# Kernel optimization log

Hardware: AMD Instinct MI355X
Metric: run time of the kernel (lower is better)

Reference implementation:

```python
import jax, jax.numpy as jnp
import numpy as np

N = 50000   # num_entities
R = 16      # num_relations
B = 8       # num_bases
D = 128     # embedding_dim == hidden_dim
E = 625000  # num_edges
EPS = 1e-5  # LayerNorm eps


def _rgcn_layer(x, row, col, edge_type, bases, coef, selfw, bias):
    # weights[r] = sum_b coef[r,b] * bases[b]  (rio). We apply bases to x first
    # (cheaper: N*B*d*d) then mix by coefficients, since (x @ W[r])[col] == x[col] @ W[r].
    z = jnp.einsum('ni,bio->bno', x, bases)          # [B,N,D]
    y = jnp.einsum('rb,bno->rno', coef, z)           # [R,N,D] == x @ W[r]
    msg = y[edge_type, col]                          # [E,D] per-edge messages
    key = edge_type * N + row                        # combined (relation,node) segment id
    agg = jax.ops.segment_sum(msg, key, num_segments=R * N).reshape(R, N, D)
    deg = jax.ops.segment_sum(jnp.ones((msg.shape[0],), x.dtype), key,
                              num_segments=R * N).reshape(R, N, 1)
    agg = (agg / jnp.maximum(deg, 1.0)).sum(0)       # per-relation mean-agg, summed over r
    return x @ selfw + agg + bias


def _layernorm(x, g, b):
    m = x.mean(-1, keepdims=True)
    v = ((x - m) ** 2).mean(-1, keepdims=True)
    return (x - m) * jax.lax.rsqrt(v + EPS) * g + b


def setup_inputs() -> dict:
    key = jax.random.key(0)
    ks = jax.random.split(key, 10)
    s = 1.0 / np.sqrt(D)
    sb = 1.0 / np.sqrt(B)
    return {
        'edge_index': jax.random.randint(ks[0], (2, E), 0, N),
        'edge_type': jax.random.randint(ks[1], (E,), 0, R),
        'emb': jax.random.normal(ks[2], (N, D), jnp.float32) * s,
        'bases1': jax.random.normal(ks[3], (B, D, D), jnp.float32) * s,
        'coef1': jax.random.normal(ks[4], (R, B), jnp.float32) * sb,
        'selfw1': jax.random.normal(ks[5], (D, D), jnp.float32) * s,
        'bias1': jnp.zeros((D,), jnp.float32),
        'g1': jnp.ones((D,), jnp.float32),
        'b1': jnp.zeros((D,), jnp.float32),
        'bases2': jax.random.normal(ks[6], (B, D, D), jnp.float32) * s,
        'coef2': jax.random.normal(ks[7], (R, B), jnp.float32) * sb,
        'selfw2': jax.random.normal(ks[8], (D, D), jnp.float32) * s,
        'bias2': jnp.zeros((D,), jnp.float32),
        'g2': jnp.ones((D,), jnp.float32),
        'b2': jnp.zeros((D,), jnp.float32),
    }


def reference(edge_index, edge_type, emb, bases1, coef1, selfw1, bias1, g1, b1,
              bases2, coef2, selfw2, bias2, g2, b2):
    row, col = edge_index[0], edge_index[1]
    x = emb
    # layer 1 (dropout is identity in eval)
    x = _rgcn_layer(x, row, col, edge_type, bases1, coef1, selfw1, bias1)
    x = jax.nn.relu(_layernorm(x, g1, b1))
    # layer 2
    x = _rgcn_layer(x, row, col, edge_type, bases2, coef2, selfw2, bias2)
    x = jax.nn.relu(_layernorm(x, g2, b2))
    return x
```

## Files before the change

### kernel.cpp

```cpp
#include <hip/hip_runtime.h>
#include <hip/hip_bf16.h>


static constexpr int kDim = 128;
static constexpr int kRel = 16;
static constexpr int kBas = 8;
static constexpr int kSeg = kBas + 1;

typedef __attribute__((ext_vector_type(8))) short bf16x8;
typedef __attribute__((ext_vector_type(4))) float f32x4;

static __device__ __forceinline__ float bf2f_rg(unsigned short h) {
    return __uint_as_float(((unsigned)h) << 16);
}
static __device__ __forceinline__ unsigned short f2bf_rg(float f) {
    unsigned u = __float_as_uint(f);
    u = u + 0x7fffu + ((u >> 16) & 1u);
    return (unsigned short)(u >> 16);
}

static __device__ __forceinline__ void gload_lds16(const void* g, void* l) {
    __builtin_amdgcn_global_load_lds(
        (const __attribute__((address_space(1))) unsigned*)g,
        (__attribute__((address_space(3))) unsigned*)l, 16, 0, 0);
}

static __device__ __forceinline__ int flag_from(const unsigned short* x, int lane) {
    unsigned e0 = ((unsigned)x[lane] >> 7) & 0xFFu;
    unsigned e1 = ((unsigned)x[lane + 64] >> 7) & 0xFFu;
    int bad = (e0 >= 0x86u) || (e1 >= 0x86u);
    return (__ballot(bad) != 0ull) ? 1 : 0;
}

__global__ void RGCNEncoder_89962384982025_kernel(unsigned* p, int n) {
    int i = blockIdx.x * 256 + threadIdx.x;
    if (i < n) p[i] = 0x3F803F80u;
}

__global__ void cvt_rg(const void* xraw, unsigned short* xout, int n) {
    __shared__ int fsh;
    if (threadIdx.x < 64) {
        int fl = flag_from((const unsigned short*)xraw, threadIdx.x);
        if (threadIdx.x == 0) fsh = fl;
    }
    __syncthreads();
    int f = fsh;
    int i = blockIdx.x * 256 + threadIdx.x;
    if (i >= n) return;
    if (f)
        xout[i] = f2bf_rg(((const float*)xraw)[i]);
    else
        xout[i] = ((const unsigned short*)xraw)[i];
}

__global__ void zero_rg(int* p, int n) {
    int i = blockIdx.x * 256 + threadIdx.x;
    if (i < n) p[i] = 0;
}

__global__ void count_rg(const int* ei, const int* et, int* cnt, int E) {
    int e = blockIdx.x * 256 + threadIdx.x;
    if (e < E) atomicAdd(&cnt[ei[e] * kRel + et[e]], 1);
}

__global__ void scanA_rg(const int* cnt, int* rowptr, int* bsum, int n) {
    __shared__ int sh[256];
    int tid = threadIdx.x;
    int i = blockIdx.x * 256 + tid;
    int v = (i < n) ? cnt[i] : 0;
    sh[tid] = v;
    __syncthreads();
    for (int off = 1; off < 256; off <<= 1) {
        int t = (tid >= off) ? sh[tid - off] : 0;
        __syncthreads();
        sh[tid] += t;
        __syncthreads();
    }
    if (i < n) rowptr[i + 1] = sh[tid];
    if (tid == 255) bsum[blockIdx.x] = sh[255];
}
__global__ void scanB_rg(int* bsum, int nb) {
    __shared__ int partial[256];
    int tid = threadIdx.x;
    int chunk = (nb + 255) / 256;
    int s0 = tid * chunk;
    int s1 = min(s0 + chunk, nb);
    int sum = 0;
    for (int i = s0; i < s1; ++i) sum += bsum[i];
    partial[tid] = sum;
    __syncthreads();
    for (int off = 1; off < 256; off <<= 1) {
        int t = (tid >= off) ? partial[tid - off] : 0;
        __syncthreads();
        partial[tid] += t;
        __syncthreads();
    }
    int run = (tid == 0) ? 0 : partial[tid - 1];
    for (int i = s0; i < s1; ++i) { int v = bsum[i]; bsum[i] = run; run += v; }
}
__global__ void scanC_rg(int* rowptr, const int* bsum, int n) {
    int i = blockIdx.x * 256 + threadIdx.x;
    if (i < n) rowptr[i + 1] += bsum[blockIdx.x];
    if (i == 0) rowptr[0] = 0;
}

__global__ void fill_rg(const int* ei, const int* et, const int* rowptr,
                        int* cnt, int* pcols, int E) {
    int e = blockIdx.x * 256 + threadIdx.x;
    if (e < E) {
        int rel = et[e];
        int key = ei[e] * kRel + rel;
        int old = atomicSub(&cnt[key], 1);
        pcols[rowptr[key] + old - 1] = ei[E + e] | (rel << 26);
    }
}

__global__ void wall_rg(const void* bases, const void* coef, const void* selfw,
                        const unsigned short* emb, unsigned short* wallT,
                        float* coefw) {
    __shared__ int fsh;
    if (threadIdx.x < 64) {
        int fl = flag_from(emb, threadIdx.x);
        if (threadIdx.x == 0) fsh = fl;
    }
    __syncthreads();
    int f = fsh;
    int idx = blockIdx.x * 256 + threadIdx.x;
    int b = idx >> 14;
    int o = (idx >> 7) & 127;
    int k = idx & 127;
    if (blockIdx.x == 0 && threadIdx.x < kRel * kBas) {
        coefw[threadIdx.x] = f ? ((const float*)coef)[threadIdx.x]
                               : bf2f_rg(((const unsigned short*)coef)[threadIdx.x]);
    }
    if (b < kBas) {
        float bv = f ? ((const float*)bases)[b * 16384 + k * 128 + o]
                     : bf2f_rg(((const unsigned short*)bases)[b * 16384 + k * 128 + o]);
        wallT[idx] = f2bf_rg(bv);
    } else {
        float sv = f ? ((const float*)selfw)[k * 128 + o]
                     : bf2f_rg(((const unsigned short*)selfw)[k * 128 + o]);
        wallT[idx] = f2bf_rg(sv);
    }
}

__global__ __launch_bounds__(256) void agg2_rg(const int* rowptr2, const int* pcols,
                                               const unsigned short* xsrc,
                                               const float* coefw,
                                               unsigned short* Gall, int N) {
    __shared__ float csh[kRel * kBas];
    if (threadIdx.x < kRel * kBas) csh[threadIdx.x] = coefw[threadIdx.x];
    __syncthreads();
    int wv = threadIdx.x >> 6;
    int lane = threadIdx.x & 63;
    int n = blockIdx.x * 4 + wv;
    if (n >= N) return;
    const int s = rowptr2[n * kRel];
    const int e = rowptr2[n * kRel + kRel];
    const unsigned short* xl = xsrc + 2 * lane;
    float g0[kBas], g1[kBas];
#pragma unroll
    for (int b = 0; b < kBas; ++b) { g0[b] = 0.f; g1[b] = 0.f; }
    float s0 = 0.f, s1 = 0.f;
    int cur = -1, cnt = 0;
    auto flush = [&]() {
        float w = __builtin_amdgcn_rcpf((float)cnt);
        float t0 = s0 * w, t1 = s1 * w;
        const float* cr = csh + cur * kBas;
#pragma unroll
        for (int b = 0; b < kBas; ++b) {
            float c = cr[b];
            g0[b] += c * t0;
            g1[b] += c * t1;
        }
        s0 = 0.f; s1 = 0.f; cnt = 0;
    };
    for (int base = s; base < e; base += 64) {
        int m = e - base;
        if (m > 64) m = 64;
        int pk = 0;
        if (base + lane < e) pk = pcols[base + lane];
        int i = 0;
        for (; i + 4 <= m; i += 4) {
            int v0 = __builtin_amdgcn_readlane(pk, i);
            int v1 = __builtin_amdgcn_readlane(pk, i + 1);
            int v2 = __builtin_amdgcn_readlane(pk, i + 2);
            int v3 = __builtin_amdgcn_readlane(pk, i + 3);
            unsigned u0 = *(const unsigned*)(xl + (size_t)(v0 & 0x03FFFFFF) * 128);
            unsigned u1 = *(const unsigned*)(xl + (size_t)(v1 & 0x03FFFFFF) * 128);
            unsigned u2 = *(const unsigned*)(xl + (size_t)(v2 & 0x03FFFFFF) * 128);
            unsigned u3 = *(const unsigned*)(xl + (size_t)(v3 & 0x03FFFFFF) * 128);
            int r0 = (int)((unsigned)v0 >> 26);
            int r1 = (int)((unsigned)v1 >> 26);
            int r2 = (int)((unsigned)v2 >> 26);
            int r3 = (int)((unsigned)v3 >> 26);
            if (r0 != cur) { if (cnt) flush(); cur = r0; }
            s0 += __uint_as_float(u0 << 16); s1 += __uint_as_float(u0 & 0xffff0000u); ++cnt;
            if (r1 != cur) { flush(); cur = r1; }
            s0 += __uint_as_float(u1 << 16); s1 += __uint_as_float(u1 & 0xffff0000u); ++cnt;
            if (r2 != cur) { flush(); cur = r2; }
            s0 += __uint_as_float(u2 << 16); s1 += __uint_as_float(u2 & 0xffff0000u); ++cnt;
            if (r3 != cur) { flush(); cur = r3; }
            s0 += __uint_as_float(u3 << 16); s1 += __uint_as_float(u3 & 0xffff0000u); ++cnt;
        }
        for (; i < m; ++i) {
            int v = __builtin_amdgcn_readlane(pk, i);
            unsigned u = *(const unsigned*)(xl + (size_t)(v & 0x03FFFFFF) * 128);
            int rel = (int)((unsigned)v >> 26);
            if (rel != cur) { if (cnt) flush(); cur = rel; }
            s0 += __uint_as_float(u << 16);
            s1 += __uint_as_float(u & 0xffff0000u);
            ++cnt;
        }
    }
    if (cnt) flush();
    unsigned short* grow = Gall + (size_t)n * (kBas * 128) + 2 * lane;
#pragma unroll
    for (int b = 0; b < kBas; ++b) {
        unsigned outp = (unsigned)f2bf_rg(g0[b]) | ((unsigned)f2bf_rg(g1[b]) << 16);
        *(unsigned*)(grow + b * 128) = outp;
    }
}

__global__ __launch_bounds__(256, 3) void fusegemm_rg(const unsigned short* Gall,
                                                      const unsigned short* x,
                                                      const unsigned short* wallT,
                                                      const void* bias, const void* gw,
                                                      const void* bw,
                                                      const unsigned short* emb,
                                                      unsigned short* out_b, float* out_f,
                                                      int ofp32, int M) {
    __shared__ __align__(16) unsigned short As[2][64][128];
    __shared__ float pS[64][5];
    __shared__ float pQ[64][5];
    __shared__ float mrs[64][2];
    __shared__ int fsh;
    const int m0 = blockIdx.x * 64;
    const int tid = threadIdx.x;
    const int wave = tid >> 6;
    const int lane = tid & 63;
    const int wn = wave * 32;
    const int lrow = lane & 15;
    const int lq = lane >> 4;
    if (tid < 64) {
        int fl = flag_from(emb, tid);
        if (tid == 0) fsh = fl;
    }

    auto stage = [&](int seg, int buf) {
        const char* srcb;
        size_t rstrideB, segoffB;
        if (seg < kBas) { srcb = (const char*)Gall; rstrideB = kBas * 256; segoffB = (size_t)seg * 256; }
        else            { srcb = (const char*)x;    rstrideB = 256;        segoffB = 0; }
#pragma unroll
        for (int it = 0; it < 4; ++it) {
            int gi = (wave * 4 + it) * 64 + lane;
            int row = gi >> 4;
            int c = ((gi & 15) << 4) ^ ((row & 7) << 4);
            int gr = m0 + row;
            if (gr > M - 1) gr = M - 1;
            const char* src = srcb + (size_t)gr * rstrideB + segoffB + (size_t)c;
            unsigned short* ldst = &As[buf][0][0] + ((wave * 4 + it) << 9);
            gload_lds16(src, ldst);
        }
    };

    f32x4 acc[4][2] = {};
    stage(0, 0);
    __syncthreads();
    int cur = 0;
    for (int seg = 0; seg < kSeg; ++seg) {
        const unsigned short* Bsrc = wallT + (size_t)seg * 16384;
        bf16x8 b[4][2];
#pragma unroll
        for (int kk4 = 0; kk4 < 4; ++kk4)
#pragma unroll
            for (int nt = 0; nt < 2; ++nt)
                b[kk4][nt] = *(const bf16x8*)(Bsrc + (size_t)(wn + nt * 16 + lrow) * 128
                                              + kk4 * 32 + lq * 8);
        __builtin_amdgcn_sched_barrier(0);
        if (seg < kSeg - 1) stage(seg + 1, cur ^ 1);
#pragma unroll
        for (int kk4 = 0; kk4 < 4; ++kk4) {
            bf16x8 a4[4];
#pragma unroll
            for (int mt = 0; mt < 4; ++mt) {
                int row = mt * 16 + lrow;
                int cb = (kk4 * 64 + lq * 16) ^ ((row & 7) << 4);
                a4[mt] = *(const bf16x8*)((const char*)&As[cur][0][0]
                                          + row * 256 + cb);
            }
#pragma unroll
            for (int mt = 0; mt < 4; ++mt)
#pragma unroll
                for (int nt = 0; nt < 2; ++nt)
                    acc[mt][nt] = __builtin_amdgcn_mfma_f32_16x16x32_bf16(
                        a4[mt], b[kk4][nt], acc[mt][nt], 0, 0, 0);
        }
        asm volatile("s_waitcnt vmcnt(0)" ::: "memory");
        __builtin_amdgcn_s_barrier();
        cur ^= 1;
    }

    const int f = fsh;
    float bv[2], gv[2], betav[2];
#pragma unroll
    for (int nt = 0; nt < 2; ++nt) {
        int gc = wn + nt * 16 + lrow;
        if (f) {
            bv[nt] = ((const float*)bias)[gc];
            gv[nt] = ((const float*)gw)[gc];
            betav[nt] = ((const float*)bw)[gc];
        } else {
            bv[nt] = bf2f_rg(((const unsigned short*)bias)[gc]);
            gv[nt] = bf2f_rg(((const unsigned short*)gw)[gc]);
            betav[nt] = bf2f_rg(((const unsigned short*)bw)[gc]);
        }
    }
#pragma unroll
    for (int mt = 0; mt < 4; ++mt)
#pragma unroll
        for (int i = 0; i < 4; ++i) {
            float sv = 0.f, qv = 0.f;
#pragma unroll
            for (int nt = 0; nt < 2; ++nt) {
                float v = acc[mt][nt][i] + bv[nt];
                acc[mt][nt][i] = v;
                sv += v;
                qv += v * v;
            }
            for (int o = 1; o < 16; o <<= 1) {
                sv += __shfl_xor(sv, o);
                qv += __shfl_xor(qv, o);
            }
            if (lrow == 0) {
                int row = mt * 16 + lq * 4 + i;
                pS[row][wave] = sv;
                pQ[row][wave] = qv;
            }
        }
    __syncthreads();
    if (tid < 64) {
        float s4 = pS[tid][0] + pS[tid][1] + pS[tid][2] + pS[tid][3];
        float q4 = pQ[tid][0] + pQ[tid][1] + pQ[tid][2] + pQ[tid][3];
        float mean = s4 * (1.0f / 128.0f);
        float var = q4 * (1.0f / 128.0f) - mean * mean;
        mrs[tid][0] = mean;
        mrs[tid][1] = rsqrtf(var + 1e-5f);
    }
    __syncthreads();
#pragma unroll
    for (int mt = 0; mt < 4; ++mt)
#pragma unroll
        for (int i = 0; i < 4; ++i) {
            int row = mt * 16 + lq * 4 + i;
            int gr = m0 + row;
            if (gr < M) {
                float mean = mrs[row][0];
                float rs = mrs[row][1];
#pragma unroll
                for (int nt = 0; nt < 2; ++nt) {
                    int gc = wn + nt * 16 + lrow;
                    float o = fmaxf((acc[mt][nt][i] - mean) * rs * gv[nt] + betav[nt], 0.f);
                    if (ofp32)
                        out_f[(size_t)gr * 128 + gc] = o;
                    else
                        out_b[(size_t)gr * 128 + gc] = f2bf_rg(o);
                }
            }
        }
}

extern "C" void kernel_launch(void* const* d_in, const int* in_sizes, int n_in,
                              void* d_out, int out_size, void* d_ws, size_t ws_size,
                              hipStream_t stream) {
    const int* ei = (const int*)d_in[0];
    const int* et = (const int*)d_in[1];
    const void* emb    = d_in[2];
    const void* bases1 = d_in[3];
    const void* coef1  = d_in[4];
    const void* selfw1 = d_in[5];
    const void* bias1  = d_in[6];
    const void* g1     = d_in[7];
    const void* b1     = d_in[8];
    const void* bases2 = d_in[9];
    const void* coef2  = d_in[10];
    const void* selfw2 = d_in[11];
    const void* bias2  = d_in[12];
    const void* g2     = d_in[13];
    const void* b2     = d_in[14];

    const int E = in_sizes[1];
    const int N = out_size / kDim;
    const int n16 = N * kRel;
    const int nsb = (n16 + 255) / 256;

    char* ws = (char*)d_ws;
    size_t off = 0;
    float* coefw = (float*)(ws + off); off += 512;
    int* rowptr2 = (int*)(ws + off); off += (((size_t)n16 + 1) * 4 + 255) & ~(size_t)255;
    int* cnt     = (int*)(ws + off); off += ((size_t)n16 * 4 + 255) & ~(size_t)255;
    int* bsum    = (int*)(ws + off); off += ((size_t)nsb * 4 + 255) & ~(size_t)255;
    int* pcols   = (int*)(ws + off); off += ((size_t)E * 4 + 255) & ~(size_t)255;
    unsigned short* wallT = (unsigned short*)(ws + off);
    off += ((size_t)kSeg * 16384 * 2 + 255) & ~(size_t)255;
    unsigned short* xin  = (unsigned short*)(ws + off);
    off += ((size_t)N * 128 * 2 + 255) & ~(size_t)255;
    unsigned short* xmid = (unsigned short*)(ws + off);
    off += ((size_t)N * 128 * 2 + 255) & ~(size_t)255;
    unsigned short* Gall = (unsigned short*)(ws + off);
    (void)n_in; (void)ws_size;

    const int eblk = (E + 255) / 256;
    const int mblk64 = (N + 63) / 64;
    const int ablk = (N + 3) / 4;
    const int nelem = N * 128;
    const unsigned short* embh = (const unsigned short*)emb;

    RGCNEncoder_89962384982025_kernel<<<1, 256, 0, stream>>>((unsigned*)d_out, 256);

    cvt_rg<<<(nelem + 255) / 256, 256, 0, stream>>>(emb, xin, nelem);

    zero_rg<<<(n16 + 255) / 256, 256, 0, stream>>>(cnt, n16);
    count_rg<<<eblk, 256, 0, stream>>>(ei, et, cnt, E);
    scanA_rg<<<nsb, 256, 0, stream>>>(cnt, rowptr2, bsum, n16);
    scanB_rg<<<1, 256, 0, stream>>>(bsum, nsb);
    scanC_rg<<<nsb, 256, 0, stream>>>(rowptr2, bsum, n16);
    fill_rg<<<eblk, 256, 0, stream>>>(ei, et, rowptr2, cnt, pcols, E);

    wall_rg<<<kSeg * 64, 256, 0, stream>>>(bases1, coef1, selfw1, embh, wallT, coefw);
    agg2_rg<<<ablk, 256, 0, stream>>>(rowptr2, pcols, xin, coefw, Gall, N);
    fusegemm_rg<<<mblk64, 256, 0, stream>>>(Gall, xin, wallT, bias1, g1, b1, embh,
                                            xmid, (float*)nullptr, 0, N);

    wall_rg<<<kSeg * 64, 256, 0, stream>>>(bases2, coef2, selfw2, embh, wallT, coefw);
    agg2_rg<<<ablk, 256, 0, stream>>>(rowptr2, pcols, xmid, coefw, Gall, N);
    fusegemm_rg<<<mblk64, 256, 0, stream>>>(Gall, xmid, wallT, bias2, g2, b2, embh,
                                            (unsigned short*)nullptr, (float*)d_out,
                                            1, N);
}
```

Baseline: 374.4 us.

## Fuse neighbor aggregation and basis GEMM into one kernel via LDS

Merges the per-node aggregation kernel and the fused GEMM+LayerNorm kernel into one 512-thread kernel per 32-node tile. Each wave aggregates four nodes and writes the per-basis sums straight into swizzled LDS, and the MFMA GEMM then reads them from there. This removes the Gall global intermediate, which costs 8x128 bf16 per node to write and read back, along with one launch per layer. In exchange the block is smaller, the gather phase is serialized within the block before the GEMM starts, and occupancy depends on the larger LDS footprint.

```diff
diff --git a/kernel.cpp b/kernel.cpp
--- a/kernel.cpp
+++ b/kernel.cpp
@@ -144,191 +144,160 @@
     }
 }
 
-__global__ __launch_bounds__(256) void agg2_rg(const int* rowptr2, const int* pcols,
-                                               const unsigned short* xsrc,
-                                               const float* coefw,
-                                               unsigned short* Gall, int N) {
+__global__ __launch_bounds__(512, 4) void aggemm_rg(const int* rowptr2, const int* pcols,
+                                                    const unsigned short* xsrc,
+                                                    const unsigned short* wallT,
+                                                    const float* coefw,
+                                                    const void* bias, const void* gw,
+                                                    const void* bw,
+                                                    const unsigned short* emb,
+                                                    unsigned short* out_b, float* out_f,
+                                                    int ofp32, int M) {
+    __shared__ __align__(16) unsigned short G[kSeg][32][128];
     __shared__ float csh[kRel * kBas];
-    if (threadIdx.x < kRel * kBas) csh[threadIdx.x] = coefw[threadIdx.x];
-    __syncthreads();
-    int wv = threadIdx.x >> 6;
-    int lane = threadIdx.x & 63;
-    int n = blockIdx.x * 4 + wv;
-    if (n >= N) return;
-    const int s = rowptr2[n * kRel];
-    const int e = rowptr2[n * kRel + kRel];
-    const unsigned short* xl = xsrc + 2 * lane;
-    float g0[kBas], g1[kBas];
-#pragma unroll
-    for (int b = 0; b < kBas; ++b) { g0[b] = 0.f; g1[b] = 0.f; }
-    float s0 = 0.f, s1 = 0.f;
-    int cur = -1, cnt = 0;
-    auto flush = [&]() {
-        float w = __builtin_amdgcn_rcpf((float)cnt);
-        float t0 = s0 * w, t1 = s1 * w;
-        const float* cr = csh + cur * kBas;
-#pragma unroll
-        for (int b = 0; b < kBas; ++b) {
-            float c = cr[b];
-            g0[b] += c * t0;
-            g1[b] += c * t1;
-        }
-        s0 = 0.f; s1 = 0.f; cnt = 0;
-    };
-    for (int base = s; base < e; base += 64) {
-        int m = e - base;
-        if (m > 64) m = 64;
-        int pk = 0;
-        if (base + lane < e) pk = pcols[base + lane];
-        int i = 0;
-        for (; i + 4 <= m; i += 4) {
-            int v0 = __builtin_amdgcn_readlane(pk, i);
-            int v1 = __builtin_amdgcn_readlane(pk, i + 1);
-            int v2 = __builtin_amdgcn_readlane(pk, i + 2);
-            int v3 = __builtin_amdgcn_readlane(pk, i + 3);
-            unsigned u0 = *(const unsigned*)(xl + (size_t)(v0 & 0x03FFFFFF) * 128);
-            unsigned u1 = *(const unsigned*)(xl + (size_t)(v1 & 0x03FFFFFF) * 128);
-            unsigned u2 = *(const unsigned*)(xl + (size_t)(v2 & 0x03FFFFFF) * 128);
-            unsigned u3 = *(const unsigned*)(xl + (size_t)(v3 & 0x03FFFFFF) * 128);
-            int r0 = (int)((unsigned)v0 >> 26);
-            int r1 = (int)((unsigned)v1 >> 26);
-            int r2 = (int)((unsigned)v2 >> 26);
-            int r3 = (int)((unsigned)v3 >> 26);
-            if (r0 != cur) { if (cnt) flush(); cur = r0; }
-            s0 += __uint_as_float(u0 << 16); s1 += __uint_as_float(u0 & 0xffff0000u); ++cnt;
-            if (r1 != cur) { flush(); cur = r1; }
-            s0 += __uint_as_float(u1 << 16); s1 += __uint_as_float(u1 & 0xffff0000u); ++cnt;
-            if (r2 != cur) { flush(); cur = r2; }
-            s0 += __uint_as_float(u2 << 16); s1 += __uint_as_float(u2 & 0xffff0000u); ++cnt;
-            if (r3 != cur) { flush(); cur = r3; }
-            s0 += __uint_as_float(u3 << 16); s1 += __uint_as_float(u3 & 0xffff0000u); ++cnt;
-        }
-        for (; i < m; ++i) {
-            int v = __builtin_amdgcn_readlane(pk, i);
-            unsigned u = *(const unsigned*)(xl + (size_t)(v & 0x03FFFFFF) * 128);
-            int rel = (int)((unsigned)v >> 26);
-            if (rel != cur) { if (cnt) flush(); cur = rel; }
-            s0 += __uint_as_float(u << 16);
-            s1 += __uint_as_float(u & 0xffff0000u);
-            ++cnt;
-        }
-    }
-    if (cnt) flush();
-    unsigned short* grow = Gall + (size_t)n * (kBas * 128) + 2 * lane;
-#pragma unroll
-    for (int b = 0; b < kBas; ++b) {
-        unsigned outp = (unsigned)f2bf_rg(g0[b]) | ((unsigned)f2bf_rg(g1[b]) << 16);
-        *(unsigned*)(grow + b * 128) = outp;
-    }
-}
-
-__global__ __launch_bounds__(256, 3) void fusegemm_rg(const unsigned short* Gall,
-                                                      const unsigned short* x,
-                                                      const unsigned short* wallT,
-                                                      const void* bias, const void* gw,
-                                                      const void* bw,
-                                                      const unsigned short* emb,
-                                                      unsigned short* out_b, float* out_f,
-                                                      int ofp32, int M) {
-    __shared__ __align__(16) unsigned short As[2][64][128];
-    __shared__ float pS[64][5];
-    __shared__ float pQ[64][5];
-    __shared__ float mrs[64][2];
+    __shared__ float pS[32][8];
+    __shared__ float pQ[32][8];
+    __shared__ float mrs[32][2];
     __shared__ int fsh;
-    const int m0 = blockIdx.x * 64;
     const int tid = threadIdx.x;
     const int wave = tid >> 6;
     const int lane = tid & 63;
-    const int wn = wave * 32;
-    const int lrow = lane & 15;
-    const int lq = lane >> 4;
+    const int m0 = blockIdx.x * 32;
     if (tid < 64) {
         int fl = flag_from(emb, tid);
         if (tid == 0) fsh = fl;
     }
-
-    auto stage = [&](int seg, int buf) {
-        const char* srcb;
-        size_t rstrideB, segoffB;
-        if (seg < kBas) { srcb = (const char*)Gall; rstrideB = kBas * 256; segoffB = (size_t)seg * 256; }
-        else            { srcb = (const char*)x;    rstrideB = 256;        segoffB = 0; }
-#pragma unroll
-        for (int it = 0; it < 4; ++it) {
-            int gi = (wave * 4 + it) * 64 + lane;
-            int row = gi >> 4;
-            int c = ((gi & 15) << 4) ^ ((row & 7) << 4);
-            int gr = m0 + row;
-            if (gr > M - 1) gr = M - 1;
-            const char* src = srcb + (size_t)gr * rstrideB + segoffB + (size_t)c;
-            unsigned short* ldst = &As[buf][0][0] + ((wave * 4 + it) << 9);
-            gload_lds16(src, ldst);
+    if (tid < kRel * kBas) csh[tid] = coefw[tid];
+
+    {
+        int row = tid >> 4;
+        int c = ((tid & 15) << 4) ^ ((row & 7) << 4);
+        int gr = m0 + row;
+        if (gr > M - 1) gr = M - 1;
+        gload_lds16((const char*)xsrc + (size_t)gr * 256 + c,
+                    &G[kBas][0][0] + tid * 8);
+    }
+    __syncthreads();
+
+    const int ln0 = wave * 4;
+    for (int j = 0; j < 4; ++j) {
+        int ln = ln0 + j;
+        int n = m0 + ln;
+        if (n >= M) break;
+        const int s = rowptr2[n * kRel];
+        const int e = rowptr2[n * kRel + kRel];
+        const unsigned short* xl = xsrc + 2 * lane;
+        float g0[kBas], g1[kBas];
+#pragma unroll
+        for (int b = 0; b < kBas; ++b) { g0[b] = 0.f; g1[b] = 0.f; }
+        float s0 = 0.f, s1 = 0.f;
+        int cur = -1, cnt = 0;
+        auto flush = [&]() {
+            float w = __builtin_amdgcn_rcpf((float)cnt);
+            float t0 = s0 * w, t1 = s1 * w;
+            const float* cr = csh + cur * kBas;
+#pragma unroll
+            for (int b = 0; b < kBas; ++b) {
+                float c = cr[b];
+                g0[b] += c * t0;
+                g1[b] += c * t1;
+            }
+            s0 = 0.f; s1 = 0.f; cnt = 0;
+        };
+        for (int base = s; base < e; base += 64) {
+            int m = e - base;
+            if (m > 64) m = 64;
+            int pk = 0;
+            if (base + lane < e) pk = pcols[base + lane];
+            int i = 0;
+            for (; i + 4 <= m; i += 4) {
+                int v0 = __builtin_amdgcn_readlane(pk, i);
+                int v1 = __builtin_amdgcn_readlane(pk, i + 1);
+                int v2 = __builtin_amdgcn_readlane(pk, i + 2);
+                int v3 = __builtin_amdgcn_readlane(pk, i + 3);
+                unsigned u0 = *(const unsigned*)(xl + (size_t)(v0 & 0x03FFFFFF) * 128);
+                unsigned u1 = *(const unsigned*)(xl + (size_t)(v1 & 0x03FFFFFF) * 128);
+                unsigned u2 = *(const unsigned*)(xl + (size_t)(v2 & 0x03FFFFFF) * 128);
+                unsigned u3 = *(const unsigned*)(xl + (size_t)(v3 & 0x03FFFFFF) * 128);
+                int r0 = (int)((unsigned)v0 >> 26);
+                int r1 = (int)((unsigned)v1 >> 26);
+                int r2 = (int)((unsigned)v2 >> 26);
+                int r3 = (int)((unsigned)v3 >> 26);
+                if (r0 != cur) { if (cnt) flush(); cur = r0; }
+                s0 += __uint_as_float(u0 << 16); s1 += __uint_as_float(u0 & 0xffff0000u); ++cnt;
+                if (r1 != cur) { flush(); cur = r1; }
+                s0 += __uint_as_float(u1 << 16); s1 += __uint_as_float(u1 & 0xffff0000u); ++cnt;
+                if (r2 != cur) { flush(); cur = r2; }
+                s0 += __uint_as_float(u2 << 16); s1 += __uint_as_float(u2 & 0xffff0000u); ++cnt;
+                if (r3 != cur) { flush(); cur = r3; }
+                s0 += __uint_as_float(u3 << 16); s1 += __uint_as_float(u3 & 0xffff0000u); ++cnt;
+            }
+            for (; i < m; ++i) {
+                int v = __builtin_amdgcn_readlane(pk, i);
+                unsigned u = *(const unsigned*)(xl + (size_t)(v & 0x03FFFFFF) * 128);
+                int rel = (int)((unsigned)v >> 26);
+                if (rel != cur) { if (cnt) flush(); cur = rel; }
+                s0 += __uint_as_float(u << 16);
+                s1 += __uint_as_float(u & 0xffff0000u);
+                ++cnt;
+            }
         }
+        if (cnt) flush();
+        int byteoff = (lane * 4) ^ ((ln & 7) << 4);
+#pragma unroll
+        for (int b = 0; b < kBas; ++b) {
+            unsigned outp = (unsigned)f2bf_rg(g0[b]) | ((unsigned)f2bf_rg(g1[b]) << 16);
+            *(unsigned*)((char*)&G[b][0][0] + ln * 256 + byteoff) = outp;
+        }
+    }
+    __syncthreads();
+
+    const int lrow = lane & 15;
+    const int lq = lane >> 4;
+    const int col = wave * 16 + lrow;
+    f32x4 acc[2] = {};
+    bf16x8 breg[2][4];
+    auto loadB = [&](int seg, bf16x8 (&b)[4]) {
+        const unsigned short* Bsrc = wallT + (size_t)seg * 16384 + (size_t)col * 128;
+#pragma unroll
+        for (int kk4 = 0; kk4 < 4; ++kk4)
+            b[kk4] = *(const bf16x8*)(Bsrc + kk4 * 32 + lq * 8);
     };
-
-    f32x4 acc[4][2] = {};
-    stage(0, 0);
-    __syncthreads();
-    int cur = 0;
+    loadB(0, breg[0]);
+#pragma unroll
     for (int seg = 0; seg < kSeg; ++seg) {
-        const unsigned short* Bsrc = wallT + (size_t)seg * 16384;
-        bf16x8 b[4][2];
-#pragma unroll
-        for (int kk4 = 0; kk4 < 4; ++kk4)
-#pragma unroll
-            for (int nt = 0; nt < 2; ++nt)
-                b[kk4][nt] = *(const bf16x8*)(Bsrc + (size_t)(wn + nt * 16 + lrow) * 128
-                                              + kk4 * 32 + lq * 8);
-        __builtin_amdgcn_sched_barrier(0);
-        if (seg < kSeg - 1) stage(seg + 1, cur ^ 1);
+        if (seg + 1 < kSeg) loadB(seg + 1, breg[(seg + 1) & 1]);
 #pragma unroll
         for (int kk4 = 0; kk4 < 4; ++kk4) {
-            bf16x8 a4[4];
-#pragma unroll
-            for (int mt = 0; mt < 4; ++mt) {
-                int row = mt * 16 + lrow;
-                int cb = (kk4 * 64 + lq * 16) ^ ((row & 7) << 4);
-                a4[mt] = *(const bf16x8*)((const char*)&As[cur][0][0]
-                                          + row * 256 + cb);
-            }
-#pragma unroll
-            for (int mt = 0; mt < 4; ++mt)
-#pragma unroll
-                for (int nt = 0; nt < 2; ++nt)
-                    acc[mt][nt] = __builtin_amdgcn_mfma_f32_16x16x32_bf16(
-                        a4[mt], b[kk4][nt], acc[mt][nt], 0, 0, 0);
+#pragma unroll
+            for (int mt = 0; mt < 2; ++mt) {
+                int r = mt * 16 + lrow;
+                int cb = (kk4 * 64 + lq * 16) ^ ((r & 7) << 4);
+                bf16x8 a = *(const bf16x8*)((const char*)&G[seg][0][0] + r * 256 + cb);
+                acc[mt] = __builtin_amdgcn_mfma_f32_16x16x32_bf16(
+                    a, breg[seg & 1][kk4], acc[mt], 0, 0, 0);
+            }
         }
-        asm volatile("s_waitcnt vmcnt(0)" ::: "memory");
-        __builtin_amdgcn_s_barrier();
-        cur ^= 1;
     }
 
     const int f = fsh;
-    float bv[2], gv[2], betav[2];
-#pragma unroll
-    for (int nt = 0; nt < 2; ++nt) {
-        int gc = wn + nt * 16 + lrow;
-        if (f) {
-            bv[nt] = ((const float*)bias)[gc];
-            gv[nt] = ((const float*)gw)[gc];
-            betav[nt] = ((const float*)bw)[gc];
-        } else {
-            bv[nt] = bf2f_rg(((const unsigned short*)bias)[gc]);
-            gv[nt] = bf2f_rg(((const unsigned short*)gw)[gc]);
-            betav[nt] = bf2f_rg(((const unsigned short*)bw)[gc]);
-        }
-    }
-#pragma unroll
-    for (int mt = 0; mt < 4; ++mt)
+    float bv, gv, betav;
+    if (f) {
+        bv = ((const float*)bias)[col];
+        gv = ((const float*)gw)[col];
+        betav = ((const float*)bw)[col];
+    } else {
+        bv = bf2f_rg(((const unsigned short*)bias)[col]);
+        gv = bf2f_rg(((const unsigned short*)gw)[col]);
+        betav = bf2f_rg(((const unsigned short*)bw)[col]);
+    }
+#pragma unroll
+    for (int mt = 0; mt < 2; ++mt)
 #pragma unroll
         for (int i = 0; i < 4; ++i) {
-            float sv = 0.f, qv = 0.f;
-#pragma unroll
-            for (int nt = 0; nt < 2; ++nt) {
-                float v = acc[mt][nt][i] + bv[nt];
-                acc[mt][nt][i] = v;
-                sv += v;
-                qv += v * v;
-            }
+            float v = acc[mt][i] + bv;
+            acc[mt][i] = v;
+            float sv = v, qv = v * v;
             for (int o = 1; o < 16; o <<= 1) {
                 sv += __shfl_xor(sv, o);
                 qv += __shfl_xor(qv, o);
@@ -340,33 +309,28 @@
             }
         }
     __syncthreads();
-    if (tid < 64) {
-        float s4 = pS[tid][0] + pS[tid][1] + pS[tid][2] + pS[tid][3];
-        float q4 = pQ[tid][0] + pQ[tid][1] + pQ[tid][2] + pQ[tid][3];
-        float mean = s4 * (1.0f / 128.0f);
-        float var = q4 * (1.0f / 128.0f) - mean * mean;
+    if (tid < 32) {
+        float s8 = 0.f, q8 = 0.f;
+#pragma unroll
+        for (int w = 0; w < 8; ++w) { s8 += pS[tid][w]; q8 += pQ[tid][w]; }
+        float mean = s8 * (1.0f / 128.0f);
+        float var = q8 * (1.0f / 128.0f) - mean * mean;
         mrs[tid][0] = mean;
         mrs[tid][1] = rsqrtf(var + 1e-5f);
     }
     __syncthreads();
 #pragma unroll
-    for (int mt = 0; mt < 4; ++mt)
+    for (int mt = 0; mt < 2; ++mt)
 #pragma unroll
         for (int i = 0; i < 4; ++i) {
             int row = mt * 16 + lq * 4 + i;
             int gr = m0 + row;
             if (gr < M) {
-                float mean = mrs[row][0];
-                float rs = mrs[row][1];
-#pragma unroll
-                for (int nt = 0; nt < 2; ++nt) {
-                    int gc = wn + nt * 16 + lrow;
-                    float o = fmaxf((acc[mt][nt][i] - mean) * rs * gv[nt] + betav[nt], 0.f);
-                    if (ofp32)
-                        out_f[(size_t)gr * 128 + gc] = o;
-                    else
-                        out_b[(size_t)gr * 128 + gc] = f2bf_rg(o);
-                }
+                float o = fmaxf((acc[mt][i] - mrs[row][0]) * mrs[row][1] * gv + betav, 0.f);
+                if (ofp32)
+                    out_f[(size_t)gr * 128 + col] = o;
+                else
+                    out_b[(size_t)gr * 128 + col] = f2bf_rg(o);
             }
         }
 }
@@ -407,13 +371,10 @@
     unsigned short* xin  = (unsigned short*)(ws + off);
     off += ((size_t)N * 128 * 2 + 255) & ~(size_t)255;
     unsigned short* xmid = (unsigned short*)(ws + off);
-    off += ((size_t)N * 128 * 2 + 255) & ~(size_t)255;
-    unsigned short* Gall = (unsigned short*)(ws + off);
     (void)n_in; (void)ws_size;
 
     const int eblk = (E + 255) / 256;
-    const int mblk64 = (N + 63) / 64;
-    const int ablk = (N + 3) / 4;
+    const int mblk32 = (N + 31) / 32;
     const int nelem = N * 128;
     const unsigned short* embh = (const unsigned short*)emb;
 
@@ -429,13 +390,13 @@
     fill_rg<<<eblk, 256, 0, stream>>>(ei, et, rowptr2, cnt, pcols, E);
 
     wall_rg<<<kSeg * 64, 256, 0, stream>>>(bases1, coef1, selfw1, embh, wallT, coefw);
-    agg2_rg<<<ablk, 256, 0, stream>>>(rowptr2, pcols, xin, coefw, Gall, N);
-    fusegemm_rg<<<mblk64, 256, 0, stream>>>(Gall, xin, wallT, bias1, g1, b1, embh,
-                                            xmid, (float*)nullptr, 0, N);
+    aggemm_rg<<<mblk32, 512, 0, stream>>>(rowptr2, pcols, xin, wallT, coefw,
+                                          bias1, g1, b1, embh,
+                                          xmid, (float*)nullptr, 0, N);
 
     wall_rg<<<kSeg * 64, 256, 0, stream>>>(bases2, coef2, selfw2, embh, wallT, coefw);
-    agg2_rg<<<ablk, 256, 0, stream>>>(rowptr2, pcols, xmid, coefw, Gall, N);
-    fusegemm_rg<<<mblk64, 256, 0, stream>>>(Gall, xmid, wallT, bias2, g2, b2, embh,
-                                            (unsigned short*)nullptr, (float*)d_out,
-                                            1, N);
-}
+    aggemm_rg<<<mblk32, 512, 0, stream>>>(rowptr2, pcols, xmid, wallT, coefw,
+                                          bias2, g2, b2, embh,
+                                          (unsigned short*)nullptr, (float*)d_out,
+                                          1, N);
+}
```

Result: slower. 435.7 us (+16.4%).
